# Performance work log

Measured on AMD Instinct MI355X. Metric: run time of the kernel, lower is better.

## Reference

```python
import jax, jax.numpy as jnp
import numpy as np

HIDDEN = 768
MLP_HIDDEN = 3072
HEADS = 12
HEAD_DIM = HIDDEN // HEADS

def setup_inputs() -> dict:
    key = jax.random.key(0)
    ks = jax.random.split(key, 12)
    s = 0.02
    return {
        "x": jax.random.normal(ks[0], (16, 1024, HIDDEN), dtype=jnp.float32),
        "ln1_g": jnp.ones((HIDDEN,), jnp.float32),
        "ln1_b": jnp.zeros((HIDDEN,), jnp.float32),
        "wq": jax.random.normal(ks[1], (HIDDEN, HIDDEN), jnp.float32) * s,
        "wk": jax.random.normal(ks[2], (HIDDEN, HIDDEN), jnp.float32) * s,
        "wv": jax.random.normal(ks[3], (HIDDEN, HIDDEN), jnp.float32) * s,
        "wo": jax.random.normal(ks[4], (HIDDEN, HIDDEN), jnp.float32) * s,
        "bo": jnp.zeros((HIDDEN,), jnp.float32),
        "ln2_g": jnp.ones((HIDDEN,), jnp.float32),
        "ln2_b": jnp.zeros((HIDDEN,), jnp.float32),
        "w1": jax.random.normal(ks[5], (HIDDEN, MLP_HIDDEN), jnp.float32) * s,
        "b1": jnp.zeros((MLP_HIDDEN,), jnp.float32),
        "w2": jax.random.normal(ks[6], (MLP_HIDDEN, HIDDEN), jnp.float32) * s,
        "b2": jnp.zeros((HIDDEN,), jnp.float32),
    }

def _layernorm(x, g, b, eps=1e-5):
    mu = jnp.mean(x, axis=-1, keepdims=True)
    var = jnp.mean(jnp.square(x - mu), axis=-1, keepdims=True)
    return (x - mu) * jax.lax.rsqrt(var + eps) * g + b

def reference(x, ln1_g, ln1_b, wq, wk, wv, wo, bo, ln2_g, ln2_b, w1, b1, w2, b2):
    b, n, _ = x.shape
    h, d = HEADS, HEAD_DIM
    scale = d ** -0.5
    # Attention branch
    xn = _layernorm(x, ln1_g, ln1_b)
    q = (xn @ wq.T).reshape(b, n, h, d).transpose(0, 2, 1, 3)  # bhnd
    k = (xn @ wk.T).reshape(b, n, h, d).transpose(0, 2, 1, 3)
    v = (xn @ wv.T).reshape(b, n, h, d).transpose(0, 2, 1, 3)
    score = jax.nn.softmax(jnp.einsum('bhif,bhjf->bhij', q, k) * scale, axis=-1)
    attn = jnp.einsum('bhij,bhjf->bihf', score, v).reshape(b, n, h * d)
    x = attn @ wo.T + bo + x
    # MLP branch
    xn = _layernorm(x, ln2_g, ln2_b)
    hdn = jax.nn.gelu(xn @ w1 + b1, approximate=False)
    x = hdn @ w2 + b2 + x
    return x
```

## Files before the change

kernel.cpp:

```cpp
#include <hip/hip_runtime.h>
#include <hip/hip_bf16.h>

#define HIDDEN 768
#define MLPH   3072
#define HEADS  12
#define HD     64
#define SEQ    1024
#define BATCH  16
#define MTOT   (BATCH*SEQ)

typedef __attribute__((ext_vector_type(8))) short  short8;
typedef __attribute__((ext_vector_type(4))) short  short4x;
typedef __attribute__((ext_vector_type(8))) __bf16 bf16x8;
typedef __attribute__((ext_vector_type(4))) float  floatx4;

#define CL2 0.18033688011112042f

__device__ inline short f2bf(float f) {
  __hip_bfloat16 h = __float2bfloat16(f);
  return *reinterpret_cast<short*>(&h);
}

__device__ inline floatx4 mfma_bf16(short8 a, short8 b, floatx4 c) {
  return __builtin_amdgcn_mfma_f32_16x16x32_bf16(
      __builtin_bit_cast(bf16x8, a), __builtin_bit_cast(bf16x8, b), c, 0, 0, 0);
}

__device__ inline void gl_lds16(const short* g, short* l) {
  __builtin_amdgcn_global_load_lds(
      (const __attribute__((address_space(1))) unsigned int*)g,
      (__attribute__((address_space(3))) unsigned int*)l, 16, 0, 0);
}

__global__ __launch_bounds__(256) void conv_weights(
    const float* __restrict__ wq, const float* __restrict__ wk,
    const float* __restrict__ wv, const float* __restrict__ wo,
    const float* __restrict__ w1, const float* __restrict__ w2,
    short* __restrict__ wqkvb, short* __restrict__ wob,
    short* __restrict__ w1t,   short* __restrict__ w2t)
{
  int i = blockIdx.x * 256 + threadIdx.x;
  const int HH = HIDDEN * HIDDEN;
  if (i < HH) {
    wqkvb[i]        = f2bf(wq[i]);
    wqkvb[HH + i]   = f2bf(wk[i]);
    wqkvb[2*HH + i] = f2bf(wv[i]);
    wob[i]          = f2bf(wo[i]);
  }
  if (i < HIDDEN * MLPH) {
    int n = i / HIDDEN, k = i % HIDDEN;
    w1t[i] = f2bf(w1[(size_t)k * MLPH + n]);
    int n2 = i / MLPH, k2 = i % MLPH;
    w2t[i] = f2bf(w2[(size_t)k2 * HIDDEN + n2]);
  }
}

__global__ __launch_bounds__(256) void ln_kernel(
    const float* __restrict__ x, const float* __restrict__ g,
    const float* __restrict__ b, short* __restrict__ out)
{
  int row = blockIdx.x;
  const float* xr = x + (size_t)row * HIDDEN;
  int t = threadIdx.x;
  float v0 = xr[t], v1 = xr[t + 256], v2 = xr[t + 512];
  float s  = v0 + v1 + v2;
  float s2 = v0*v0 + v1*v1 + v2*v2;
  for (int off = 32; off > 0; off >>= 1) {
    s  += __shfl_down(s, off);
    s2 += __shfl_down(s2, off);
  }
  __shared__ float red[8];
  __shared__ float stats[2];
  int wave = t >> 6;
  if ((t & 63) == 0) { red[wave] = s; red[4 + wave] = s2; }
  __syncthreads();
  if (t == 0) {
    float S  = red[0] + red[1] + red[2] + red[3];
    float S2 = red[4] + red[5] + red[6] + red[7];
    float mu  = S * (1.0f / HIDDEN);
    float var = S2 * (1.0f / HIDDEN) - mu * mu;
    stats[0] = mu;
    stats[1] = rsqrtf(var + 1e-5f);
  }
  __syncthreads();
  float mu = stats[0], rs = stats[1];
  short* orow = out + (size_t)row * HIDDEN;
  orow[t]       = f2bf((v0 - mu) * rs * g[t]       + b[t]);
  orow[t + 256] = f2bf((v1 - mu) * rs * g[t + 256] + b[t + 256]);
  orow[t + 512] = f2bf((v2 - mu) * rs * g[t + 512] + b[t + 512]);
}

template<int OUTMODE , bool BIAS, bool GELU_E, bool RES,
         bool SCALEQ = false>
__global__ __launch_bounds__(512, 2) void gemm_bt2(
    const short* __restrict__ A, const short* __restrict__ B,
    const float* __restrict__ bias, const float* __restrict__ res,
    void* __restrict__ out, int M, int N, int K)
{
  __shared__ alignas(16) short As[2][2][8192];
  __shared__ alignas(16) short Bs[2][2][8192];

  int tid = threadIdx.x;
  int lane = tid & 63, wave = tid >> 6;
  int wr = wave >> 2, wc = wave & 3;
  int quad = lane >> 4, lc = lane & 15;

  int nbx = gridDim.x;
  int nwg = nbx * gridDim.y;
  int orig = blockIdx.y * nbx + blockIdx.x;
  int q8 = nwg >> 3, r8 = nwg & 7;
  int xcd = orig & 7, sub = orig >> 3;
  int wg = (xcd < r8 ? xcd * (q8 + 1) : r8 * (q8 + 1) + (xcd - r8) * q8) + sub;
  int m0 = (wg / nbx) * 256;
  int n0 = (wg % nbx) * 256;

  int srow = tid >> 2;
  int skb  = (tid & 3) ^ ((srow >> 1) & 3);
  const short* ga = A + (size_t)(m0 + srow) * K + skb * 8;
  const short* gb = B + (size_t)(n0 + srow) * K + skb * 8;
  const size_t rowskip = (size_t)128 * K;
  int lb0 = wave * 512;

#define STAGE_R(MAT, gp, sl, ks, kt) {                         \
    const short* _g = (gp) + (size_t)(kt) * 64 + (ks) * 32;    \
    gl_lds16(_g,           &MAT[sl][ks][lb0]);                 \
    gl_lds16(_g + rowskip, &MAT[sl][ks][4096 + lb0]);          \
  }

  floatx4 acc[8][4];
#pragma unroll
  for (int i = 0; i < 8; ++i)
#pragma unroll
    for (int j = 0; j < 4; ++j) acc[i][j] = floatx4{0.f, 0.f, 0.f, 0.f};

  int apos = (quad ^ ((lc >> 1) & 3)) * 8;
#define RD(buf, r) (*(const short8*)&(buf)[(r) * 32 + apos])
#define MM4x4(IOFF)                                                     \
    _Pragma("unroll")                                                   \
    for (int i = 0; i < 4; ++i)                                         \
      _Pragma("unroll")                                                 \
      for (int j = 0; j < 4; ++j)                                       \
        acc[i + IOFF][j] = mfma_bf16(aF[i], bF[j], acc[i + IOFF][j]);

  int NK = K >> 6;

  STAGE_R(As, ga, 0, 0, 0); STAGE_R(Bs, gb, 0, 0, 0);
  STAGE_R(As, ga, 0, 1, 0); STAGE_R(Bs, gb, 0, 1, 0);

  for (int kt = 0; kt < NK; ++kt) {
    const int sl = kt & 1;
    const short (*as_)[8192] = As[sl];
    const short (*bs_)[8192] = Bs[sl];
    const int s2 = sl ^ 1;
    const bool st = (kt + 1 < NK);
    short8 aF[4], bF[4];

    asm volatile("s_waitcnt vmcnt(2)" ::: "memory");
    __builtin_amdgcn_s_barrier();
    asm volatile("" ::: "memory");
#pragma unroll
    for (int i = 0; i < 4; ++i) aF[i] = RD(as_[0], wr * 128 + i * 16 + lc);
#pragma unroll
    for (int j = 0; j < 4; ++j) bF[j] = RD(bs_[0], wc * 64 + j * 16 + lc);
    if (st) STAGE_R(Bs, gb, s2, 1, kt + 1);
    asm volatile("s_waitcnt lgkmcnt(0)" ::: "memory");
    __builtin_amdgcn_sched_barrier(0);
    __builtin_amdgcn_s_setprio(1);
    MM4x4(0);
    __builtin_amdgcn_s_setprio(0);

    __builtin_amdgcn_s_barrier();
    asm volatile("" ::: "memory");
#pragma unroll
    for (int i = 0; i < 4; ++i) aF[i] = RD(as_[0], wr * 128 + (i + 4) * 16 + lc);
    if (st) STAGE_R(Bs, gb, s2, 0, kt + 1);
    asm volatile("s_waitcnt lgkmcnt(0)" ::: "memory");
    __builtin_amdgcn_sched_barrier(0);
    __builtin_amdgcn_s_setprio(1);
    MM4x4(4);
    __builtin_amdgcn_s_setprio(0);

    if (st) asm volatile("s_waitcnt vmcnt(4)" ::: "memory");
    else    asm volatile("s_waitcnt vmcnt(0)" ::: "memory");
    __builtin_amdgcn_s_barrier();
    asm volatile("" ::: "memory");
#pragma unroll
    for (int i = 0; i < 4; ++i) aF[i] = RD(as_[1], wr * 128 + i * 16 + lc);
#pragma unroll
    for (int j = 0; j < 4; ++j) bF[j] = RD(bs_[1], wc * 64 + j * 16 + lc);
    if (st) STAGE_R(As, ga, s2, 0, kt + 1);
    asm volatile("s_waitcnt lgkmcnt(0)" ::: "memory");
    __builtin_amdgcn_sched_barrier(0);
    __builtin_amdgcn_s_setprio(1);
    MM4x4(0);
    __builtin_amdgcn_s_setprio(0);

    __builtin_amdgcn_s_barrier();
    asm volatile("" ::: "memory");
#pragma unroll
    for (int i = 0; i < 4; ++i) aF[i] = RD(as_[1], wr * 128 + (i + 4) * 16 + lc);
    if (st) STAGE_R(As, ga, s2, 1, kt + 1);
    asm volatile("s_waitcnt lgkmcnt(0)" ::: "memory");
    __builtin_amdgcn_sched_barrier(0);
    __builtin_amdgcn_s_setprio(1);
    MM4x4(4);
    __builtin_amdgcn_s_setprio(0);
  }
#undef STAGE_R
#undef RD
#undef MM4x4

#pragma unroll
  for (int i = 0; i < 8; ++i)
#pragma unroll
    for (int j = 0; j < 4; ++j)
#pragma unroll
      for (int r = 0; r < 4; ++r) {
        int row = m0 + wr * 128 + i * 16 + quad * 4 + r;
        int col = n0 + wc * 64 + j * 16 + lc;
        float v = acc[i][j][r];
        if (BIAS)   v += bias[col];
        if (GELU_E) v = 0.5f * v * (1.0f + erff(v * 0.70710678118f));
        if (RES)    v += res[(size_t)row * N + col];
        if (SCALEQ && col < HIDDEN) v *= CL2;
        if (OUTMODE == 1) ((short*)out)[(size_t)row * N + col] = f2bf(v);
        else              ((float*)out)[(size_t)row * N + col] = v;
      }
}

__global__ __launch_bounds__(256) void vtrans_kernel(
    const short* __restrict__ qkv, short* __restrict__ vtg)
{
  int kt = blockIdx.x, h = blockIdx.y, b = blockIdx.z;
  int t = threadIdx.x;
  __shared__ short Vl[64][72];
  const short* vb = qkv + (size_t)(b * SEQ + kt * 64) * 2304 + 1536 + h * 64;
  int row = t >> 2, seg = t & 3;
  short8 r0 = *(const short8*)(vb + (size_t)row * 2304 + seg * 16);
  short8 r1 = *(const short8*)(vb + (size_t)row * 2304 + seg * 16 + 8);
  *(short8*)&Vl[row][seg * 16]     = r0;
  *(short8*)&Vl[row][seg * 16 + 8] = r1;
  __syncthreads();
  int ks = t >> 7, d = (t & 127) >> 1, hb = t & 1;
  short8 w0;
#pragma unroll
  for (int u = 0; u < 8; ++u) {
    int blk = hb * 2 + (u >> 3), j = u & 7;
    int ksrc = ks * 32 + (blk ^ ((d >> 1) & 3)) * 8 + j;
    w0[u] = Vl[ksrc][d];
  }
  short8 w1;
#pragma unroll
  for (int u = 8; u < 16; ++u) {
    int blk = hb * 2 + (u >> 3), j = u & 7;
    int ksrc = ks * 32 + (blk ^ ((d >> 1) & 3)) * 8 + j;
    w1[u - 8] = Vl[ksrc][d];
  }
  short* o = vtg + ((size_t)((b * HEADS + h) * 16 + kt)) * 4096 + t * 16;
  *(short8*)o       = w0;
  *(short8*)(o + 8) = w1;
}

__global__ __launch_bounds__(512) void attn_kernel(
    const short* __restrict__ qkv, const short* __restrict__ vtg,
    short* __restrict__ out)
{
  int qt = blockIdx.x;
  int h  = blockIdx.y;
  int b  = blockIdx.z;
  int tid = threadIdx.x, lane = tid & 63, wave = tid >> 6;
  int quad = lane >> 4, lc = lane & 15;

  __shared__ alignas(16) short Qs[2 * 128 * 32];
  __shared__ alignas(16) short Ks[2 * 64 * 32];
  __shared__ alignas(16) short Vs[2 * 64 * 32];
  __shared__ alignas(16) short Ps[8][16 * 72];

  const int LDQ = 3 * HIDDEN;
  const short* qb = qkv + (size_t)(b * SEQ) * LDQ + h * HD;
  const short* kb = qb + HIDDEN;
  const short* vt = vtg + (size_t)((b * HEADS + h) * 16) * 4096;

  {
    int row = tid >> 2, blk = tid & 3;
    int kblk = blk ^ ((row >> 1) & 3);
#pragma unroll
    for (int t = 0; t < 2; ++t) {
      const short* g = qb + (size_t)(qt * 128 + row) * LDQ + t * 32 + kblk * 8;
      gl_lds16(g, &Qs[t * 4096 + wave * 512]);
    }
  }
  __syncthreads();

  int pos = quad ^ ((lc >> 1) & 3);
  short8 aq[2];
#pragma unroll
  for (int ks = 0; ks < 2; ++ks)
    aq[ks] = *(const short8*)&Qs[ks * 4096 + (wave * 16 + lc) * 32 + pos * 8];

  floatx4 oacc[4];
#pragma unroll
  for (int n2 = 0; n2 < 4; ++n2) oacc[n2] = floatx4{0.f, 0.f, 0.f, 0.f};
  float lsum = 0.f;

  int srow = (tid >> 2) & 63;
  int sks  = tid >> 8;
  int skb  = (tid & 3) ^ ((srow >> 1) & 3);
  const short* kg0 = kb + (size_t)srow * LDQ + sks * 32 + skb * 8;
  const short* vg0 = vt + tid * 8;
  short* pw = &Ps[wave][0];

  for (int kt = 0; kt < 16; ++kt) {
    gl_lds16(kg0 + (size_t)(kt * 64) * LDQ, &Ks[wave * 512]);
    gl_lds16(vg0 + kt * 4096, &Vs[wave * 512]);
    __syncthreads();

    floatx4 sacc[4];
#pragma unroll
    for (int m2 = 0; m2 < 4; ++m2) sacc[m2] = floatx4{0.f, 0.f, 0.f, 0.f};
#pragma unroll
    for (int ks = 0; ks < 2; ++ks) {
#pragma unroll
      for (int m2 = 0; m2 < 4; ++m2) {
        short8 ak = *(const short8*)&Ks[ks * 2048 + (m2 * 16 + lc) * 32 + pos * 8];
        sacc[m2] = mfma_bf16(ak, aq[ks], sacc[m2]);
      }
    }

#pragma unroll
    for (int m2 = 0; m2 < 4; ++m2) {
      float p0 = exp2f(sacc[m2][0]);
      float p1 = exp2f(sacc[m2][1]);
      float p2 = exp2f(sacc[m2][2]);
      float p3 = exp2f(sacc[m2][3]);
      lsum += (p0 + p1) + (p2 + p3);
      short4x pk;
      pk[0] = f2bf(p0); pk[1] = f2bf(p1); pk[2] = f2bf(p2); pk[3] = f2bf(p3);
      *(short4x*)&pw[lc * 72 + m2 * 16 + quad * 4] = pk;
    }
    asm volatile("s_waitcnt lgkmcnt(0)" ::: "memory");
    __builtin_amdgcn_sched_barrier(0);

#pragma unroll
    for (int ks = 0; ks < 2; ++ks) {
      short8 ap = *(const short8*)&pw[lc * 72 + (ks * 4 + quad) * 8];
#pragma unroll
      for (int n2 = 0; n2 < 4; ++n2) {
        short8 bv = *(const short8*)&Vs[ks * 2048 + (n2 * 16 + lc) * 32 + pos * 8];
        oacc[n2] = mfma_bf16(ap, bv, oacc[n2]);
      }
    }
    __syncthreads();
  }

  float rs = lsum;
  rs += __shfl_xor(rs, 16);
  rs += __shfl_xor(rs, 32);
#pragma unroll
  for (int r = 0; r < 4; ++r) {
    float inv = 1.0f / __shfl(rs, quad * 4 + r);
    int row = b * SEQ + qt * 128 + wave * 16 + quad * 4 + r;
#pragma unroll
    for (int n2 = 0; n2 < 4; ++n2) {
      int col = h * HD + n2 * 16 + lc;
      out[(size_t)row * HIDDEN + col] = f2bf(oacc[n2][r] * inv);
    }
  }
}

extern "C" void kernel_launch(void* const* d_in, const int* in_sizes, int n_in,
                              void* d_out, int out_size, void* d_ws, size_t ws_size,
                              hipStream_t stream) {
  const float* x    = (const float*)d_in[0];
  const float* ln1g = (const float*)d_in[1];
  const float* ln1b = (const float*)d_in[2];
  const float* wq   = (const float*)d_in[3];
  const float* wk   = (const float*)d_in[4];
  const float* wv   = (const float*)d_in[5];
  const float* wo   = (const float*)d_in[6];
  const float* bo   = (const float*)d_in[7];
  const float* ln2g = (const float*)d_in[8];
  const float* ln2b = (const float*)d_in[9];
  const float* w1   = (const float*)d_in[10];
  const float* b1   = (const float*)d_in[11];
  const float* w2   = (const float*)d_in[12];
  const float* b2   = (const float*)d_in[13];

  auto rup = [](size_t b) { return (b + 255) & ~(size_t)255; };
  const size_t wbytes = rup((size_t)3 * HIDDEN * HIDDEN * 2) +
                        rup((size_t)HIDDEN * HIDDEN * 2) +
                        rup((size_t)MLPH * HIDDEN * 2) +
                        rup((size_t)HIDDEN * MLPH * 2);

  int R = SEQ;
  const int cands[4] = {16384, 8192, 4096, 2048};
  for (int i = 0; i < 4; ++i) {
    size_t need = wbytes + rup((size_t)cands[i] * 1536) + rup((size_t)cands[i] * 6144)
                         + rup((size_t)cands[i] * 1536);
    if (need <= ws_size) { R = cands[i]; break; }
  }

  char* ws = (char*)d_ws;
  size_t off = 0;
  auto alloc = [&](size_t bytes) {
    char* p = ws + off;
    off += (bytes + 255) & ~(size_t)255;
    return p;
  };
  short* wqkvb = (short*)alloc((size_t)3 * HIDDEN * HIDDEN * 2);
  short* wob   = (short*)alloc((size_t)HIDDEN * HIDDEN * 2);
  short* w1t   = (short*)alloc((size_t)MLPH * HIDDEN * 2);
  short* w2t   = (short*)alloc((size_t)HIDDEN * MLPH * 2);
  short* slotA = (short*)alloc((size_t)R * 1536);
  short* bigR  = (short*)alloc((size_t)R * 6144);
  short* vtg   = (short*)alloc((size_t)R * 1536);

  conv_weights<<<(HIDDEN * MLPH + 255) / 256, 256, 0, stream>>>(
      wq, wk, wv, wo, w1, w2, wqkvb, wob, w1t, w2t);

  const int nch = MTOT / R;
  for (int c = 0; c < nch; ++c) {
    const float* xc  = x + (size_t)c * R * HIDDEN;
    float*       x2c = (float*)d_out + (size_t)c * R * HIDDEN;

    ln_kernel<<<R, 256, 0, stream>>>(xc, ln1g, ln1b, slotA);
    gemm_bt2<1, false, false, false, true>
        <<<dim3((3 * HIDDEN) / 256, R / 256), 512, 0, stream>>>(
        slotA, wqkvb, nullptr, nullptr, bigR, R, 3 * HIDDEN, HIDDEN);
    vtrans_kernel<<<dim3(16, HEADS, R / SEQ), 256, 0, stream>>>(bigR, vtg);
    attn_kernel<<<dim3(SEQ / 128, HEADS, R / SEQ), 512, 0, stream>>>(
        bigR, vtg, slotA);
    gemm_bt2<0, true, false, true>
        <<<dim3(HIDDEN / 256, R / 256), 512, 0, stream>>>(
        slotA, wob, bo, xc, x2c, R, HIDDEN, HIDDEN);
    ln_kernel<<<R, 256, 0, stream>>>(x2c, ln2g, ln2b, slotA);
    gemm_bt2<1, true, true, false>
        <<<dim3(MLPH / 256, R / 256), 512, 0, stream>>>(
        slotA, w1t, b1, nullptr, bigR, R, MLPH, HIDDEN);
    gemm_bt2<0, true, false, true>
        <<<dim3(HIDDEN / 256, R / 256), 512, 0, stream>>>(
        bigR, w2t, b2, x2c, x2c, R, HIDDEN, MLPH);
  }
}
```

Measured before the change: 598.9 us.

## Merge GEMM sub-phases into two barrier phases and use tanh GELU

The bf16 MFMA GEMM main loop goes from four barrier-separated sub-steps per K tile to two. Each phase issues the next tile's global-to-LDS loads for B or A, loads all 8 A fragments plus 4 B fragments, and runs the full 8x4 MFMA block. The explicit lgkmcnt waits, sched_barrier and setprio hints are removed. This halves the number of workgroup barriers, at the cost of more live fragment registers and less control over how LDS reads interleave with MFMAs. Separately, the exact erf GELU epilogue is replaced by a tanh-form approximation built from exp2 and rcp intrinsics, which is cheaper to compute but differs slightly from the reference's exact GELU.

```diff
diff --git a/kernel.cpp b/kernel.cpp
--- a/kernel.cpp
+++ b/kernel.cpp
@@ -30,6 +30,13 @@
   __builtin_amdgcn_global_load_lds(
       (const __attribute__((address_space(1))) unsigned int*)g,
       (__attribute__((address_space(3))) unsigned int*)l, 16, 0, 0);
+}
+
+__device__ inline float gelu_f(float x) {
+  float z = 0.7978845608028654f * (x + 0.044715f * x * x * x);
+  float e = __builtin_amdgcn_exp2f(z * 2.8853900817779268f);
+  float t = 1.0f - 2.0f * __builtin_amdgcn_rcpf(e + 1.0f);
+  return 0.5f * x * (1.0f + t);
 }
 
 __global__ __launch_bounds__(256) void conv_weights(
@@ -135,80 +142,52 @@
 
   int apos = (quad ^ ((lc >> 1) & 3)) * 8;
 #define RD(buf, r) (*(const short8*)&(buf)[(r) * 32 + apos])
-#define MM4x4(IOFF)                                                     \
-    _Pragma("unroll")                                                   \
-    for (int i = 0; i < 4; ++i)                                         \
-      _Pragma("unroll")                                                 \
-      for (int j = 0; j < 4; ++j)                                       \
-        acc[i + IOFF][j] = mfma_bf16(aF[i], bF[j], acc[i + IOFF][j]);
 
   int NK = K >> 6;
 
-  STAGE_R(As, ga, 0, 0, 0); STAGE_R(Bs, gb, 0, 0, 0);
-  STAGE_R(As, ga, 0, 1, 0); STAGE_R(Bs, gb, 0, 1, 0);
+  STAGE_R(Bs, gb, 0, 1, 0); STAGE_R(Bs, gb, 0, 0, 0);
+  STAGE_R(As, ga, 0, 0, 0); STAGE_R(As, ga, 0, 1, 0);
 
   for (int kt = 0; kt < NK; ++kt) {
-    const int sl = kt & 1;
-    const short (*as_)[8192] = As[sl];
-    const short (*bs_)[8192] = Bs[sl];
-    const int s2 = sl ^ 1;
+    const int sl = kt & 1, s2 = sl ^ 1;
     const bool st = (kt + 1 < NK);
-    short8 aF[4], bF[4];
+    const short* a0 = As[sl][0];
+    const short* a1 = As[sl][1];
+    const short* b0 = Bs[sl][0];
+    const short* b1 = Bs[sl][1];
+    short8 aF[8], bF[4];
 
     asm volatile("s_waitcnt vmcnt(2)" ::: "memory");
     __builtin_amdgcn_s_barrier();
     asm volatile("" ::: "memory");
-#pragma unroll
-    for (int i = 0; i < 4; ++i) aF[i] = RD(as_[0], wr * 128 + i * 16 + lc);
-#pragma unroll
-    for (int j = 0; j < 4; ++j) bF[j] = RD(bs_[0], wc * 64 + j * 16 + lc);
-    if (st) STAGE_R(Bs, gb, s2, 1, kt + 1);
-    asm volatile("s_waitcnt lgkmcnt(0)" ::: "memory");
-    __builtin_amdgcn_sched_barrier(0);
-    __builtin_amdgcn_s_setprio(1);
-    MM4x4(0);
-    __builtin_amdgcn_s_setprio(0);
-
-    __builtin_amdgcn_s_barrier();
-    asm volatile("" ::: "memory");
-#pragma unroll
-    for (int i = 0; i < 4; ++i) aF[i] = RD(as_[0], wr * 128 + (i + 4) * 16 + lc);
-    if (st) STAGE_R(Bs, gb, s2, 0, kt + 1);
-    asm volatile("s_waitcnt lgkmcnt(0)" ::: "memory");
-    __builtin_amdgcn_sched_barrier(0);
-    __builtin_amdgcn_s_setprio(1);
-    MM4x4(4);
-    __builtin_amdgcn_s_setprio(0);
+    if (st) { STAGE_R(Bs, gb, s2, 1, kt + 1); STAGE_R(Bs, gb, s2, 0, kt + 1); }
+#pragma unroll
+    for (int j = 0; j < 4; ++j) bF[j] = RD(b0, wc * 64 + j * 16 + lc);
+#pragma unroll
+    for (int i = 0; i < 8; ++i) aF[i] = RD(a0, wr * 128 + i * 16 + lc);
+#pragma unroll
+    for (int i = 0; i < 8; ++i)
+#pragma unroll
+      for (int j = 0; j < 4; ++j)
+        acc[i][j] = mfma_bf16(aF[i], bF[j], acc[i][j]);
 
     if (st) asm volatile("s_waitcnt vmcnt(4)" ::: "memory");
     else    asm volatile("s_waitcnt vmcnt(0)" ::: "memory");
     __builtin_amdgcn_s_barrier();
     asm volatile("" ::: "memory");
-#pragma unroll
-    for (int i = 0; i < 4; ++i) aF[i] = RD(as_[1], wr * 128 + i * 16 + lc);
-#pragma unroll
-    for (int j = 0; j < 4; ++j) bF[j] = RD(bs_[1], wc * 64 + j * 16 + lc);
-    if (st) STAGE_R(As, ga, s2, 0, kt + 1);
-    asm volatile("s_waitcnt lgkmcnt(0)" ::: "memory");
-    __builtin_amdgcn_sched_barrier(0);
-    __builtin_amdgcn_s_setprio(1);
-    MM4x4(0);
-    __builtin_amdgcn_s_setprio(0);
-
-    __builtin_amdgcn_s_barrier();
-    asm volatile("" ::: "memory");
-#pragma unroll
-    for (int i = 0; i < 4; ++i) aF[i] = RD(as_[1], wr * 128 + (i + 4) * 16 + lc);
-    if (st) STAGE_R(As, ga, s2, 1, kt + 1);
-    asm volatile("s_waitcnt lgkmcnt(0)" ::: "memory");
-    __builtin_amdgcn_sched_barrier(0);
-    __builtin_amdgcn_s_setprio(1);
-    MM4x4(4);
-    __builtin_amdgcn_s_setprio(0);
+    if (st) { STAGE_R(As, ga, s2, 0, kt + 1); STAGE_R(As, ga, s2, 1, kt + 1); }
+#pragma unroll
+    for (int j = 0; j < 4; ++j) bF[j] = RD(b1, wc * 64 + j * 16 + lc);
+#pragma unroll
+    for (int i = 0; i < 8; ++i) aF[i] = RD(a1, wr * 128 + i * 16 + lc);
+#pragma unroll
+    for (int i = 0; i < 8; ++i)
+#pragma unroll
+      for (int j = 0; j < 4; ++j)
+        acc[i][j] = mfma_bf16(aF[i], bF[j], acc[i][j]);
   }
 #undef STAGE_R
 #undef RD
-#undef MM4x4
 
 #pragma unroll
   for (int i = 0; i < 8; ++i)
@@ -220,7 +199,7 @@
         int col = n0 + wc * 64 + j * 16 + lc;
         float v = acc[i][j][r];
         if (BIAS)   v += bias[col];
-        if (GELU_E) v = 0.5f * v * (1.0f + erff(v * 0.70710678118f));
+        if (GELU_E) v = gelu_f(v);
         if (RES)    v += res[(size_t)row * N + col];
         if (SCALEQ && col < HIDDEN) v *= CL2;
         if (OUTMODE == 1) ((short*)out)[(size_t)row * N + col] = f2bf(v);
```

Result: slower. 673.5 us (+12.5%).
